# Performance work log

Measured on AMD Instinct MI355X. Metric: run time of the kernel, lower is better.

Reference implementation:

```python
import jax, jax.numpy as jnp
import numpy as np

N_NODES = 50000   # hypergraph nodes
N_EDGES = 20000   # hyperedges
M = 400000        # node-edge incidences (node copies)
L = 800000        # inner GIN graph edges per side
HID = 128
IN_DIM = 128
B = 32            # graphs in batch
C = 10            # num_classes
N_LAYERS = 2
INNER = 2         # inner_num_layers
BN_EPS = 1e-5


def setup_inputs() -> dict:
    key = jax.random.key(0)
    ks = jax.random.split(key, 16)
    s = 0.05
    inp = {}
    inp["x_N"] = jax.random.normal(ks[0], (N_NODES, IN_DIM), jnp.float32)
    # embedding linear
    inp["We"] = jax.random.normal(ks[1], (IN_DIM, HID), jnp.float32) * s
    inp["be"] = jnp.zeros((HID,), jnp.float32)
    # GIN params: [outer_layer, direction(N2E/E2N), inner_conv, mlp_linear, hid, hid]
    inp["Wg"] = jax.random.normal(ks[2], (N_LAYERS, 2, INNER, 2, HID, HID), jnp.float32) * s
    inp["bg"] = jnp.zeros((N_LAYERS, 2, INNER, 2, HID), jnp.float32)
    inp["eps_g"] = jnp.zeros((N_LAYERS, 2, INNER), jnp.float32)
    # eval-mode BatchNorm affine params per inner conv
    inp["gamma"] = jnp.ones((N_LAYERS, 2, INNER, HID), jnp.float32)
    inp["beta"] = jnp.zeros((N_LAYERS, 2, INNER, HID), jnp.float32)
    # per-layer prediction heads
    inp["Wp"] = jax.random.normal(ks[3], (N_LAYERS + 1, HID, C), jnp.float32) * s
    inp["bp"] = jnp.zeros((N_LAYERS + 1, C), jnp.float32)
    # index tensors
    inp["ori_node_idx"] = jax.random.randint(ks[4], (M,), 0, N_NODES)
    inp["node2edge"] = jax.random.randint(ks[5], (M,), 0, N_EDGES)
    inp["edge_index_N"] = jax.random.randint(ks[6], (2, L), 0, M)
    inp["ori_edge_idx"] = jax.random.randint(ks[7], (M,), 0, N_EDGES)
    inp["edge2node"] = jax.random.randint(ks[8], (M,), 0, N_NODES)
    inp["edge_index_E"] = jax.random.randint(ks[9], (2, L), 0, M)
    inp["batch"] = jax.random.randint(ks[10], (M,), 0, B)
    return inp


def _gin(x, src, dst, Wg, bg, eps, gamma, beta):
    # GIN over the copy graph: h = MLP((1+eps)*x + sum_{j->i} x_j), BN (eval), ReLU between convs
    inv_std = 1.0 / jnp.sqrt(1.0 + BN_EPS)
    n = x.shape[0]
    for l in range(INNER):
        agg = jax.ops.segment_sum(x[src], dst, num_segments=n)
        h = (1.0 + eps[l]) * x + agg
        h = jax.nn.relu(h @ Wg[l, 0] + bg[l, 0])
        h = h @ Wg[l, 1] + bg[l, 1]
        h = gamma[l] * h * inv_std + beta[l]
        x = jax.nn.relu(h) if l < INNER - 1 else h
    return x


def reference(x_N, We, be, Wg, bg, eps_g, gamma, beta, Wp, bp,
              ori_node_idx, node2edge, edge_index_N,
              ori_edge_idx, edge2node, edge_index_E, batch):
    node_x = x_N @ We + be                       # [N, HID]
    xs = [node_x]
    for i in range(N_LAYERS):
        # node -> edge: gather copies, inner GIN, segment-sum pool over hyperedges
        nx = node_x[ori_node_idx]                # [M, HID]
        nx = _gin(nx, edge_index_N[0], edge_index_N[1],
                  Wg[i, 0], bg[i, 0], eps_g[i, 0], gamma[i, 0], beta[i, 0])
        edge_x = jax.ops.segment_sum(nx, node2edge, num_segments=N_EDGES)
        edge_x = jax.nn.relu(edge_x)             # EdgeUpdate (dropout off in eval)
        # edge -> node
        ex = edge_x[ori_edge_idx]                # [M, HID]
        ex = _gin(ex, edge_index_E[0], edge_index_E[1],
                  Wg[i, 1], bg[i, 1], eps_g[i, 1], gamma[i, 1], beta[i, 1])
        node_x = jax.ops.segment_sum(ex, edge2node, num_segments=N_NODES)
        node_x = jax.nn.relu(node_x)             # NodeUpdate
        xs.append(node_x)
    score = jnp.zeros((B, C), x_N.dtype)
    for i, x in enumerate(xs):
        pooled = jax.ops.segment_sum(x[ori_node_idx], batch, num_segments=B)
        score = score + pooled @ Wp[i] + bp[i]
    return score
```

## Files before the change

kernel.cpp:

```cpp
#include <hip/hip_runtime.h>
#include <hip/hip_bf16.h>

#define HID 128
static const int N_NODES = 50000;
static const int N_EDGES = 20000;
static const int M_COPIES = 400000;
static const int L_EDGES = 800000;
static const int NBATCH = 32;
static const int NCLS = 10;
#define INV_STD 0.9999950000374997f
#define IDX_CAP 384
#define POOL_CAP 2048

typedef __attribute__((ext_vector_type(4))) float f32x4;
typedef __attribute__((ext_vector_type(8))) short short8;
typedef __attribute__((ext_vector_type(8))) unsigned short ushort8;
typedef __attribute__((ext_vector_type(4))) unsigned short u16x4;

__device__ __forceinline__ float bf2f(unsigned short u) {
    union { unsigned u; float f; } v; v.u = ((unsigned)u) << 16; return v.f;
}
__device__ __forceinline__ unsigned short f2bf(float f) {
    union { float f; unsigned u; } v; v.f = f;
    unsigned r = v.u + 0x7FFFu + ((v.u >> 16) & 1u);
    return (unsigned short)(r >> 16);
}
__device__ __forceinline__ void gatomic_add(float* p, float v) {
    unsafeAtomicAdd(p, v);
}

template<int H>
__device__ __forceinline__ void mfma_quarter(const unsigned short* Ws, const short8* xv,
                                             f32x4* acc, int quad, int ln) {
#pragma unroll
    for (int kc = 0; kc < 4; ++kc) {
#pragma unroll
        for (int tt = 0; tt < 2; ++tt) {
            short8 wa = *(const short8*)(Ws + (((kc * 4 + quad) * 32) + tt * 16 + ln) * 8);
            acc[H * 2 + tt] = __builtin_amdgcn_mfma_f32_16x16x32_bf16(wa, xv[kc], acc[H * 2 + tt], 0, 0, 0);
        }
    }
}

__global__ __launch_bounds__(256) void prep_w(const float* __restrict__ We,
                                              const float* __restrict__ Wg,
                                              unsigned short* __restrict__ Wt) {
    int t = blockIdx.x * 256 + threadIdx.x;
    if (t >= 17 * 16384) return;
    int mat = t >> 14, rem = t & 16383;
    int n = rem >> 7, k = rem & 127;
    const float* src = (mat == 0) ? We : (Wg + (size_t)(mat - 1) * 16384);
    Wt[t] = f2bf(src[k * 128 + n]);
}

__global__ __launch_bounds__(256) void hist_k(const int* __restrict__ idx, int n,
                                              int* __restrict__ cnt) {
    int t = blockIdx.x * 256 + threadIdx.x;
    if (t < n) atomicAdd(&cnt[idx[t]], 1);
}

__global__ __launch_bounds__(256) void scan1_k(int* __restrict__ a, int n,
                                               int* __restrict__ part) {
    __shared__ int s[256];
    int i = blockIdx.x * 256 + threadIdx.x;
    int v = (i < n) ? a[i] : 0;
    s[threadIdx.x] = v;
    __syncthreads();
#pragma unroll
    for (int d = 1; d < 256; d <<= 1) {
        int t = (threadIdx.x >= d) ? s[threadIdx.x - d] : 0;
        __syncthreads();
        s[threadIdx.x] += t;
        __syncthreads();
    }
    if (i < n) a[i] = s[threadIdx.x] - v;
    if (threadIdx.x == 255) part[blockIdx.x] = s[255];
}

__global__ __launch_bounds__(256) void scan2_k(int* __restrict__ part, int nb) {
    __shared__ int s[256];
    __shared__ int carry;
    if (threadIdx.x == 0) carry = 0;
    __syncthreads();
    for (int base = 0; base < nb; base += 256) {
        int i = base + threadIdx.x;
        int v = (i < nb) ? part[i] : 0;
        s[threadIdx.x] = v;
        __syncthreads();
#pragma unroll
        for (int d = 1; d < 256; d <<= 1) {
            int t = (threadIdx.x >= d) ? s[threadIdx.x - d] : 0;
            __syncthreads();
            s[threadIdx.x] += t;
            __syncthreads();
        }
        if (i < nb) part[i] = carry + s[threadIdx.x] - v;
        __syncthreads();
        if (threadIdx.x == 0) carry += s[255];
        __syncthreads();
    }
}

__global__ __launch_bounds__(256) void scan3_k(int* __restrict__ a, int n,
                                               const int* __restrict__ part) {
    int i = blockIdx.x * 256 + threadIdx.x;
    if (i < n) a[i] += part[blockIdx.x];
}

__global__ __launch_bounds__(256) void fill_edge_k(
    const int* __restrict__ src, const int* __restrict__ dst,
    const int* __restrict__ remap, int n, int* __restrict__ off,
    int* __restrict__ srcs, int* __restrict__ comps) {
    int e = blockIdx.x * 256 + threadIdx.x;
    if (e >= n) return;
    int d = dst[e];
    int pos = atomicAdd(&off[d], 1);
    int s = src[e];
    srcs[pos] = s;
    comps[pos] = remap[s];
}

__global__ __launch_bounds__(256) void fill_pool_k(
    const int* __restrict__ seg, int n, int* __restrict__ off,
    int* __restrict__ items) {
    int m = blockIdx.x * 256 + threadIdx.x;
    if (m >= n) return;
    int pos = atomicAdd(&off[seg[m]], 1);
    items[pos] = m;
}

__global__ __launch_bounds__(256) void segsum_pool(
    const unsigned* __restrict__ tbl, const int* __restrict__ off,
    const int* __restrict__ items, unsigned* __restrict__ out, int nseg)
{
    __shared__ int sIdx[POOL_CAP];
    int tid = threadIdx.x;
    int wave = tid >> 6, lane = tid & 63;
    int s0 = blockIdx.x * 16;
    int sN = min(s0 + 16, nseg);
    int bstart = (s0 == 0) ? 0 : off[s0 - 1];
    int bend = off[sN - 1];
    int cnt = bend - bstart;
    bool useLds = (cnt <= POOL_CAP);
    if (useLds)
        for (int i = tid; i < cnt; i += 256) sIdx[i] = items[bstart + i];
    __syncthreads();

    int mb = s0 + wave * 4;
    float a0[4] = {0.f, 0.f, 0.f, 0.f}, a1[4] = {0.f, 0.f, 0.f, 0.f};
    int pos[4], end[4];
#pragma unroll
    for (int i = 0; i < 4; ++i) {
        int m = mb + i;
        if (m < nseg) { pos[i] = (m == 0) ? 0 : off[m - 1]; end[i] = off[m]; }
        else { pos[i] = 0; end[i] = 0; }
    }
    bool more = (pos[0] < end[0]) | (pos[1] < end[1]) | (pos[2] < end[2]) | (pos[3] < end[3]);
    while (more) {
        more = false;
        unsigned v[4]; bool ld[4];
#pragma unroll
        for (int i = 0; i < 4; ++i) {
            ld[i] = pos[i] < end[i];
            if (ld[i]) {
                int r = useLds ? sIdx[pos[i] - bstart] : items[pos[i]];
                v[i] = tbl[(size_t)r * 64 + lane];
            }
        }
#pragma unroll
        for (int i = 0; i < 4; ++i) if (ld[i]) {
            a0[i] += bf2f((unsigned short)(v[i] & 0xffffu));
            a1[i] += bf2f((unsigned short)(v[i] >> 16));
            ++pos[i];
            more = more || (pos[i] < end[i]);
        }
    }
#pragma unroll
    for (int i = 0; i < 4; ++i) {
        int m = mb + i;
        if (m < nseg) {
            float r0 = fmaxf(a0[i], 0.f), r1 = fmaxf(a1[i], 0.f);
            out[(size_t)m * 64 + lane] = (unsigned)f2bf(r0) | ((unsigned)f2bf(r1) << 16);
        }
    }
}

template<bool CONV0>
__global__ __launch_bounds__(256, 6) void fused_conv(
    const unsigned short* __restrict__ tbl,
    const int* __restrict__ self_idx,
    const int* __restrict__ off, const int* __restrict__ items,
    const float* __restrict__ eps_ptr,
    const unsigned short* __restrict__ W1t, const float* __restrict__ b1,
    const unsigned short* __restrict__ W2t, const float* __restrict__ b2,
    const float* __restrict__ gam, const float* __restrict__ bet,
    unsigned short* __restrict__ out)
{
    __shared__ __align__(16) unsigned short Xs[16 * 64 * 8];
    __shared__ __align__(16) unsigned short Ws[16 * 32 * 8];
    __shared__ int sIdx[IDX_CAP];
    __shared__ int meta[192];
    const int tid = threadIdx.x;
    const int row0 = blockIdx.x * 64;

    const int bstart = (row0 == 0) ? 0 : off[row0 - 1];
    const int cnt = off[row0 + 63] - bstart;
    const bool useLds = (cnt <= IDX_CAP);

    if (tid < 64) {
        int gr = row0 + tid;
        meta[tid]       = (gr == 0) ? 0 : off[gr - 1];
        meta[64 + tid]  = off[gr];
        meta[128 + tid] = CONV0 ? self_idx[gr] : gr;
    }
#pragma unroll
    for (int i = 0; i < 2; ++i) {
        int chunk = tid + i * 256;
        int n = chunk >> 4, gg = chunk & 15;
        *(short8*)(Ws + (gg * 32 + n) * 8) = *(const short8*)(W1t + n * 128 + gg * 8);
    }
    if (useLds)
        for (int i = tid; i < cnt; i += 256) sIdx[i] = items[bstart + i];
    __syncthreads();

    const float e = 1.0f + eps_ptr[0];
    const int g = tid & 15;
    const int rb = tid >> 4;
#pragma unroll
    for (int i = 0; i < 4; ++i) {
        int r = rb + 16 * i;
        int start = meta[r], end = meta[64 + r], self = meta[128 + r];
        float a[8];
        ushort8 u = *(const ushort8*)(tbl + (size_t)self * 128 + g * 8);
#pragma unroll
        for (int j = 0; j < 8; ++j) a[j] = e * bf2f(u[j]);
        if (useLds) {
            int pos = start - bstart, pe = end - bstart;
            for (; pos + 2 <= pe; pos += 2) {
                int i0 = sIdx[pos], i1 = sIdx[pos + 1];
                ushort8 v0 = *(const ushort8*)(tbl + (size_t)i0 * 128 + g * 8);
                ushort8 v1 = *(const ushort8*)(tbl + (size_t)i1 * 128 + g * 8);
#pragma unroll
                for (int j = 0; j < 8; ++j) a[j] += bf2f(v0[j]) + bf2f(v1[j]);
            }
            if (pos < pe) {
                int i0 = sIdx[pos];
                ushort8 v0 = *(const ushort8*)(tbl + (size_t)i0 * 128 + g * 8);
#pragma unroll
                for (int j = 0; j < 8; ++j) a[j] += bf2f(v0[j]);
            }
        } else {
            for (int pos = start; pos < end; ++pos) {
                int rr = items[pos];
                ushort8 v = *(const ushort8*)(tbl + (size_t)rr * 128 + g * 8);
#pragma unroll
                for (int j = 0; j < 8; ++j) a[j] += bf2f(v[j]);
            }
        }
        ushort8 xv;
#pragma unroll
        for (int j = 0; j < 8; ++j) xv[j] = f2bf(a[j]);
        *(ushort8*)(Xs + (g * 64 + r) * 8) = xv;
    }
    __syncthreads();

    const int lane = tid & 63;
    const int ln = lane & 15, quad = lane >> 4;
    const int row = (tid >> 6) * 16 + ln;

    short8 xb[4];
#pragma unroll
    for (int kc = 0; kc < 4; ++kc)
        xb[kc] = *(const short8*)(Xs + ((kc * 4 + quad) * 64 + row) * 8);

    f32x4 acc[8];
#pragma unroll
    for (int t = 0; t < 8; ++t) acc[t] = (f32x4){0.f, 0.f, 0.f, 0.f};

    mfma_quarter<0>(Ws, xb, acc, quad, ln);
#pragma unroll
    for (int h = 1; h < 4; ++h) {
        __syncthreads();
#pragma unroll
        for (int i = 0; i < 2; ++i) {
            int chunk = tid + i * 256;
            int n = chunk >> 4, gg = chunk & 15;
            *(short8*)(Ws + (gg * 32 + n) * 8) = *(const short8*)(W1t + (h * 32 + n) * 128 + gg * 8);
        }
        __syncthreads();
        if (h == 1) mfma_quarter<1>(Ws, xb, acc, quad, ln);
        else if (h == 2) mfma_quarter<2>(Ws, xb, acc, quad, ln);
        else mfma_quarter<3>(Ws, xb, acc, quad, ln);
    }
    {
        const int j0 = (quad & 1) * 4;
#pragma unroll
        for (int t = 0; t < 8; ++t) {
            int p0 = t * 16 + quad * 4;
            f32x4 bv = *(const f32x4*)(b1 + p0);
            u16x4 hp;
#pragma unroll
            for (int i = 0; i < 4; ++i) hp[i] = f2bf(fmaxf(acc[t][i] + bv[i], 0.f));
            *(u16x4*)(Xs + ((p0 >> 3) * 64 + row) * 8 + j0) = hp;
        }
    }
    __syncthreads();
#pragma unroll
    for (int i = 0; i < 2; ++i) {
        int chunk = tid + i * 256;
        int n = chunk >> 4, gg = chunk & 15;
        *(short8*)(Ws + (gg * 32 + n) * 8) = *(const short8*)(W2t + n * 128 + gg * 8);
    }
    __syncthreads();

    short8 hb[4];
#pragma unroll
    for (int kc = 0; kc < 4; ++kc)
        hb[kc] = *(const short8*)(Xs + ((kc * 4 + quad) * 64 + row) * 8);

#pragma unroll
    for (int t = 0; t < 8; ++t) acc[t] = (f32x4){0.f, 0.f, 0.f, 0.f};

    mfma_quarter<0>(Ws, hb, acc, quad, ln);
#pragma unroll
    for (int h = 1; h < 4; ++h) {
        __syncthreads();
#pragma unroll
        for (int i = 0; i < 2; ++i) {
            int chunk = tid + i * 256;
            int n = chunk >> 4, gg = chunk & 15;
            *(short8*)(Ws + (gg * 32 + n) * 8) = *(const short8*)(W2t + (h * 32 + n) * 128 + gg * 8);
        }
        __syncthreads();
        if (h == 1) mfma_quarter<1>(Ws, hb, acc, quad, ln);
        else if (h == 2) mfma_quarter<2>(Ws, hb, acc, quad, ln);
        else mfma_quarter<3>(Ws, hb, acc, quad, ln);
    }

    const int m = row0 + row;
#pragma unroll
    for (int t = 0; t < 8; ++t) {
        int n0 = t * 16 + quad * 4;
        f32x4 bv = *(const f32x4*)(b2 + n0);
        f32x4 gv = *(const f32x4*)(gam + n0);
        f32x4 tv = *(const f32x4*)(bet + n0);
        u16x4 op;
#pragma unroll
        for (int i = 0; i < 4; ++i) {
            float h = acc[t][i] + bv[i];
            h = gv[i] * h * INV_STD + tv[i];
            if (CONV0) h = fmaxf(h, 0.f);
            op[i] = f2bf(h);
        }
        *(u16x4*)(out + (size_t)m * 128 + n0) = op;
    }
}

__global__ __launch_bounds__(256) void gemm_embed(
    const float* __restrict__ in, const unsigned short* __restrict__ Wt,
    const float* __restrict__ bias, unsigned short* __restrict__ out_bf, int rows)
{
    __shared__ __align__(16) unsigned short Xs[16 * 64 * 8];
    __shared__ __align__(16) unsigned short Ws[16 * 128 * 8];
    int tid = threadIdx.x;
    int row0 = blockIdx.x * 64;
#pragma unroll
    for (int i = 0; i < 8; ++i) {
        int chunk = tid + i * 256;
        int n = chunk >> 4, g = chunk & 15;
        *(short8*)(Ws + (g * 128 + n) * 8) = *(const short8*)(Wt + n * 128 + g * 8);
    }
#pragma unroll
    for (int i = 0; i < 4; ++i) {
        int chunk = tid + i * 256;
        int r = chunk >> 4, g = chunk & 15;
        int gr = row0 + r;
        ushort8 v;
        if (gr < rows) {
            const float* p = in + (size_t)gr * 128 + g * 8;
            f32x4 a0 = *(const f32x4*)p;
            f32x4 a1 = *(const f32x4*)(p + 4);
#pragma unroll
            for (int j = 0; j < 4; ++j) { v[j] = f2bf(a0[j]); v[4 + j] = f2bf(a1[j]); }
        } else {
#pragma unroll
            for (int j = 0; j < 8; ++j) v[j] = 0;
        }
        *(ushort8*)(Xs + (g * 64 + r) * 8) = v;
    }
    __syncthreads();
    int wave = tid >> 6, lane = tid & 63;
    int m0 = wave * 16;
    int ln = lane & 15, quad = lane >> 4;
    f32x4 acc[8];
#pragma unroll
    for (int t = 0; t < 8; ++t) acc[t] = (f32x4){0.f, 0.f, 0.f, 0.f};
#pragma unroll
    for (int kc = 0; kc < 4; ++kc) {
        int g = kc * 4 + quad;
        short8 a = *(const short8*)(Xs + (g * 64 + m0 + ln) * 8);
#pragma unroll
        for (int t = 0; t < 8; ++t) {
            short8 b = *(const short8*)(Ws + (g * 128 + t * 16 + ln) * 8);
            acc[t] = __builtin_amdgcn_mfma_f32_16x16x32_bf16(a, b, acc[t], 0, 0, 0);
        }
    }
#pragma unroll
    for (int t = 0; t < 8; ++t) {
        int col = t * 16 + ln;
        float bi = bias[col];
#pragma unroll
        for (int i = 0; i < 4; ++i) {
            int gr = row0 + m0 + quad * 4 + i;
            if (gr < rows) out_bf[(size_t)gr * 128 + col] = f2bf(acc[t][i] + bi);
        }
    }
}

template<bool ACCUM>
__global__ __launch_bounds__(256) void proj_y(
    const unsigned short* __restrict__ nx, const float* __restrict__ Wp,
    float* __restrict__ y, int rows)
{
    __shared__ float Wl[HID * NCLS];
    for (int i = threadIdx.x; i < HID * NCLS; i += 256) Wl[i] = Wp[i];
    __syncthreads();
    int r = blockIdx.x * 256 + threadIdx.x;
    if (r >= rows) return;
    float acc[NCLS];
#pragma unroll
    for (int c = 0; c < NCLS; ++c) acc[c] = 0.f;
    const unsigned short* xp = nx + (size_t)r * 128;
#pragma unroll 4
    for (int g = 0; g < 16; ++g) {
        ushort8 u = *(const ushort8*)(xp + g * 8);
#pragma unroll
        for (int j = 0; j < 8; ++j) {
            float xv = bf2f(u[j]);
            const float* w = Wl + (g * 8 + j) * NCLS;
#pragma unroll
            for (int c = 0; c < NCLS; ++c) acc[c] += xv * w[c];
        }
    }
    float* yp = y + (size_t)r * NCLS;
#pragma unroll
    for (int c = 0; c < NCLS; ++c) {
        if (ACCUM) yp[c] += acc[c];
        else yp[c] = acc[c];
    }
}

__global__ __launch_bounds__(256) void score_scatter(
    const float* __restrict__ y, const int* __restrict__ ori,
    const int* __restrict__ batch, float* __restrict__ score)
{
    __shared__ float sc[NBATCH * NCLS];
    for (int i = threadIdx.x; i < NBATCH * NCLS; i += 256) sc[i] = 0.f;
    __syncthreads();
    int stride = gridDim.x * 256;
    for (int m = blockIdx.x * 256 + threadIdx.x; m < M_COPIES; m += stride) {
        int r = ori[m], b = batch[m];
        const float* yp = y + (size_t)r * NCLS;
#pragma unroll
        for (int c = 0; c < NCLS; ++c)
            __hip_atomic_fetch_add(&sc[b * NCLS + c], yp[c],
                                   __ATOMIC_RELAXED, __HIP_MEMORY_SCOPE_WORKGROUP);
    }
    __syncthreads();
    for (int i = threadIdx.x; i < NBATCH * NCLS; i += 256) gatomic_add(score + i, sc[i]);
}

__global__ void score_final(const float* __restrict__ score, const float* __restrict__ bp,
                            float* __restrict__ out)
{
    int t = threadIdx.x;
    if (t >= NBATCH * NCLS) return;
    int c = t % NCLS;
    out[t] = score[t] + bp[c] + bp[NCLS + c] + bp[2 * NCLS + c];
}

__global__ void fill_sentinel(float* out, int n, float enc) {
    int t = blockIdx.x * 64 + threadIdx.x;
    if (t < n) out[t] = enc;
}

static inline void build_csr_edge(const int* src, const int* dst, const int* remap,
                                  int nitem, int nseg, int* off, int* part,
                                  int* srcs, int* comps, hipStream_t stream) {
    int nb = (nseg + 255) / 256;
    (void)hipMemsetAsync(off, 0, (size_t)nseg * 4, stream);
    hist_k<<<(nitem + 255) / 256, 256, 0, stream>>>(dst, nitem, off);
    scan1_k<<<nb, 256, 0, stream>>>(off, nseg, part);
    scan2_k<<<1, 256, 0, stream>>>(part, nb);
    scan3_k<<<nb, 256, 0, stream>>>(off, nseg, part);
    fill_edge_k<<<(nitem + 255) / 256, 256, 0, stream>>>(src, dst, remap, nitem, off, srcs, comps);
}
static inline void build_csr_pool(const int* seg, int nitem, int nseg,
                                  int* off, int* part, int* items, hipStream_t stream) {
    int nb = (nseg + 255) / 256;
    (void)hipMemsetAsync(off, 0, (size_t)nseg * 4, stream);
    hist_k<<<(nitem + 255) / 256, 256, 0, stream>>>(seg, nitem, off);
    scan1_k<<<nb, 256, 0, stream>>>(off, nseg, part);
    scan2_k<<<1, 256, 0, stream>>>(part, nb);
    scan3_k<<<nb, 256, 0, stream>>>(off, nseg, part);
    fill_pool_k<<<(nitem + 255) / 256, 256, 0, stream>>>(seg, nitem, off, items);
}

extern "C" void kernel_launch(void* const* d_in, const int* in_sizes, int n_in,
                              void* d_out, int out_size, void* d_ws, size_t ws_size,
                              hipStream_t stream) {
    const float* x_N    = (const float*)d_in[0];
    const float* We     = (const float*)d_in[1];
    const float* be     = (const float*)d_in[2];
    const float* Wg     = (const float*)d_in[3];
    const float* bg     = (const float*)d_in[4];
    const float* eps_g  = (const float*)d_in[5];
    const float* gam    = (const float*)d_in[6];
    const float* bet    = (const float*)d_in[7];
    const float* Wp     = (const float*)d_in[8];
    const float* bp     = (const float*)d_in[9];
    const int* ori_node = (const int*)d_in[10];
    const int* node2edge= (const int*)d_in[11];
    const int* eiN      = (const int*)d_in[12];
    const int* ori_edge = (const int*)d_in[13];
    const int* edge2node= (const int*)d_in[14];
    const int* eiE      = (const int*)d_in[15];
    const int* batch    = (const int*)d_in[16];

    char* p = (char*)d_ws;
    auto take = [&](size_t n) { char* r = p; p += (n + 255) & ~(size_t)255; return r; };
    unsigned short* Wt  = (unsigned short*)take((size_t)17 * 16384 * 2);
    unsigned short* Xb  = (unsigned short*)take((size_t)M_COPIES * 128 * 2);
    unsigned short* Xb2 = (unsigned short*)take((size_t)M_COPIES * 128 * 2);
    unsigned short* nx  = (unsigned short*)take((size_t)N_NODES * 128 * 2);
    unsigned short* ex  = (unsigned short*)take((size_t)N_EDGES * 128 * 2);
    float* y            = (float*)take((size_t)N_NODES * NCLS * 4);
    float* score        = (float*)take((size_t)NBATCH * NCLS * 4);
    int* offN           = (int*)take((size_t)M_COPIES * 4);
    int* offE           = (int*)take((size_t)M_COPIES * 4);
    int* off_n2e        = (int*)take((size_t)N_EDGES * 4);
    int* off_e2n        = (int*)take((size_t)N_NODES * 4);
    int* srcsN          = (int*)take((size_t)L_EDGES * 4);
    int* compsN         = (int*)take((size_t)L_EDGES * 4);
    int* srcsE          = (int*)take((size_t)L_EDGES * 4);
    int* compsE         = (int*)take((size_t)L_EDGES * 4);
    int* it_n2e         = (int*)take((size_t)M_COPIES * 4);
    int* it_e2n         = (int*)take((size_t)M_COPIES * 4);
    int* part           = (int*)take((size_t)2048 * 4);
    size_t need = (size_t)(p - (char*)d_ws);
    if (need > ws_size) {
        fill_sentinel<<<(out_size + 63) / 64, 64, 0, stream>>>(
            (float*)d_out, out_size, 1.0e9f + (float)ws_size);
        return;
    }

    prep_w<<<1088, 256, 0, stream>>>(We, Wg, Wt);
    (void)hipMemsetAsync(score, 0, (size_t)NBATCH * NCLS * 4, stream);

    build_csr_edge(eiN, eiN + L_EDGES, ori_node, L_EDGES, M_COPIES, offN, part, srcsN, compsN, stream);
    build_csr_edge(eiE, eiE + L_EDGES, ori_edge, L_EDGES, M_COPIES, offE, part, srcsE, compsE, stream);
    build_csr_pool(node2edge, M_COPIES, N_EDGES, off_n2e, part, it_n2e, stream);
    build_csr_pool(edge2node, M_COPIES, N_NODES, off_e2n, part, it_e2n, stream);

    gemm_embed<<<(N_NODES + 63) / 64, 256, 0, stream>>>(x_N, Wt, be, nx, N_NODES);
    proj_y<false><<<(N_NODES + 255) / 256, 256, 0, stream>>>(nx, Wp, y, N_NODES);

    const int MBLK = M_COPIES / 64;
    for (int layer = 0; layer < 2; ++layer) {
        for (int dir = 0; dir < 2; ++dir) {
            int cj0 = layer * 4 + dir * 2;
            int cj1 = cj0 + 1;
            const unsigned short* base = (dir == 0) ? nx : ex;
            const int* selfI = (dir == 0) ? ori_node : ori_edge;
            const int* offD  = (dir == 0) ? offN : offE;
            const int* srcsD = (dir == 0) ? srcsN : srcsE;
            const int* compD = (dir == 0) ? compsN : compsE;

            fused_conv<true><<<MBLK, 256, 0, stream>>>(
                base, selfI, offD, compD, eps_g + cj0,
                Wt + (size_t)(1 + cj0 * 2) * 16384, bg + (cj0 * 2) * 128,
                Wt + (size_t)(1 + cj0 * 2 + 1) * 16384, bg + (cj0 * 2 + 1) * 128,
                gam + cj0 * 128, bet + cj0 * 128, Xb);
            fused_conv<false><<<MBLK, 256, 0, stream>>>(
                Xb, nullptr, offD, srcsD, eps_g + cj1,
                Wt + (size_t)(1 + cj1 * 2) * 16384, bg + (cj1 * 2) * 128,
                Wt + (size_t)(1 + cj1 * 2 + 1) * 16384, bg + (cj1 * 2 + 1) * 128,
                gam + cj1 * 128, bet + cj1 * 128, Xb2);
            if (dir == 0) {
                segsum_pool<<<(N_EDGES + 15) / 16, 256, 0, stream>>>(
                    (const unsigned*)Xb2, off_n2e, it_n2e, (unsigned*)ex, N_EDGES);
            } else {
                segsum_pool<<<(N_NODES + 15) / 16, 256, 0, stream>>>(
                    (const unsigned*)Xb2, off_e2n, it_e2n, (unsigned*)nx, N_NODES);
                proj_y<true><<<(N_NODES + 255) / 256, 256, 0, stream>>>(
                    nx, Wp + (layer + 1) * HID * NCLS, y, N_NODES);
            }
        }
    }
    score_scatter<<<256, 256, 0, stream>>>(y, ori_node, batch, score);
    score_final<<<1, 320, 0, stream>>>(score, bp, (float*)d_out);
}
```

Before: 1.636 ms.

## Halve weight LDS tile in fused conv and rewrite segment pooling per-wave

The fused GIN conv kernel now stages weights in 16-column eighths instead of 32-column quarters. That halves the weight LDS buffer and raises the launch-bounds occupancy hint from 6 to 7 blocks, at the cost of twice as many barrier-separated reload steps. The segment-sum pooling kernel is rewritten so each wave owns one segment: four sub-groups stride over its items with 16-byte vector loads, then reduce with cross-lane shuffles. This drops the LDS index staging and the serial four-segment loop, aiming for better memory parallelism in the gather.

```diff
diff --git a/kernel.cpp b/kernel.cpp
--- a/kernel.cpp
+++ b/kernel.cpp
@@ -10,7 +10,6 @@
 static const int NCLS = 10;
 #define INV_STD 0.9999950000374997f
 #define IDX_CAP 384
-#define POOL_CAP 2048
 
 typedef __attribute__((ext_vector_type(4))) float f32x4;
 typedef __attribute__((ext_vector_type(8))) short short8;
@@ -30,15 +29,12 @@
 }
 
 template<int H>
-__device__ __forceinline__ void mfma_quarter(const unsigned short* Ws, const short8* xv,
-                                             f32x4* acc, int quad, int ln) {
+__device__ __forceinline__ void mfma_eighth(const unsigned short* Ws, const short8* xv,
+                                            f32x4* acc, int quad, int ln) {
 #pragma unroll
     for (int kc = 0; kc < 4; ++kc) {
-#pragma unroll
-        for (int tt = 0; tt < 2; ++tt) {
-            short8 wa = *(const short8*)(Ws + (((kc * 4 + quad) * 32) + tt * 16 + ln) * 8);
-            acc[H * 2 + tt] = __builtin_amdgcn_mfma_f32_16x16x32_bf16(wa, xv[kc], acc[H * 2 + tt], 0, 0, 0);
-        }
+        short8 wa = *(const short8*)(Ws + (((kc * 4 + quad) * 16) + ln) * 8);
+        acc[H] = __builtin_amdgcn_mfma_f32_16x16x32_bf16(wa, xv[kc], acc[H], 0, 0, 0);
     }
 }
 
@@ -130,63 +126,37 @@
 }
 
 __global__ __launch_bounds__(256) void segsum_pool(
-    const unsigned* __restrict__ tbl, const int* __restrict__ off,
-    const int* __restrict__ items, unsigned* __restrict__ out, int nseg)
+    const unsigned short* __restrict__ tbl, const int* __restrict__ off,
+    const int* __restrict__ items, unsigned short* __restrict__ out, int nseg)
 {
-    __shared__ int sIdx[POOL_CAP];
-    int tid = threadIdx.x;
-    int wave = tid >> 6, lane = tid & 63;
-    int s0 = blockIdx.x * 16;
-    int sN = min(s0 + 16, nseg);
-    int bstart = (s0 == 0) ? 0 : off[s0 - 1];
-    int bend = off[sN - 1];
-    int cnt = bend - bstart;
-    bool useLds = (cnt <= POOL_CAP);
-    if (useLds)
-        for (int i = tid; i < cnt; i += 256) sIdx[i] = items[bstart + i];
-    __syncthreads();
-
-    int mb = s0 + wave * 4;
-    float a0[4] = {0.f, 0.f, 0.f, 0.f}, a1[4] = {0.f, 0.f, 0.f, 0.f};
-    int pos[4], end[4];
-#pragma unroll
-    for (int i = 0; i < 4; ++i) {
-        int m = mb + i;
-        if (m < nseg) { pos[i] = (m == 0) ? 0 : off[m - 1]; end[i] = off[m]; }
-        else { pos[i] = 0; end[i] = 0; }
-    }
-    bool more = (pos[0] < end[0]) | (pos[1] < end[1]) | (pos[2] < end[2]) | (pos[3] < end[3]);
-    while (more) {
-        more = false;
-        unsigned v[4]; bool ld[4];
-#pragma unroll
-        for (int i = 0; i < 4; ++i) {
-            ld[i] = pos[i] < end[i];
-            if (ld[i]) {
-                int r = useLds ? sIdx[pos[i] - bstart] : items[pos[i]];
-                v[i] = tbl[(size_t)r * 64 + lane];
-            }
-        }
-#pragma unroll
-        for (int i = 0; i < 4; ++i) if (ld[i]) {
-            a0[i] += bf2f((unsigned short)(v[i] & 0xffffu));
-            a1[i] += bf2f((unsigned short)(v[i] >> 16));
-            ++pos[i];
-            more = more || (pos[i] < end[i]);
-        }
-    }
-#pragma unroll
-    for (int i = 0; i < 4; ++i) {
-        int m = mb + i;
-        if (m < nseg) {
-            float r0 = fmaxf(a0[i], 0.f), r1 = fmaxf(a1[i], 0.f);
-            out[(size_t)m * 64 + lane] = (unsigned)f2bf(r0) | ((unsigned)f2bf(r1) << 16);
-        }
+    int wave = threadIdx.x >> 6, lane = threadIdx.x & 63;
+    int seg = blockIdx.x * 4 + wave;
+    if (seg >= nseg) return;
+    int start = (seg == 0) ? 0 : off[seg - 1];
+    int end = off[seg];
+    int g = lane & 15, sub = lane >> 4;
+    float a[8] = {0.f, 0.f, 0.f, 0.f, 0.f, 0.f, 0.f, 0.f};
+    for (int p = start + sub; p < end; p += 4) {
+        int r = items[p];
+        ushort8 v = *(const ushort8*)(tbl + (size_t)r * 128 + g * 8);
+#pragma unroll
+        for (int j = 0; j < 8; ++j) a[j] += bf2f(v[j]);
+    }
+#pragma unroll
+    for (int j = 0; j < 8; ++j) {
+        a[j] += __shfl_xor(a[j], 16, 64);
+        a[j] += __shfl_xor(a[j], 32, 64);
+    }
+    if (sub == 0) {
+        ushort8 ov;
+#pragma unroll
+        for (int j = 0; j < 8; ++j) ov[j] = f2bf(fmaxf(a[j], 0.f));
+        *(ushort8*)(out + (size_t)seg * 128 + g * 8) = ov;
     }
 }
 
 template<bool CONV0>
-__global__ __launch_bounds__(256, 6) void fused_conv(
+__global__ __launch_bounds__(256, 7) void fused_conv(
     const unsigned short* __restrict__ tbl,
     const int* __restrict__ self_idx,
     const int* __restrict__ off, const int* __restrict__ items,
@@ -197,7 +167,7 @@
     unsigned short* __restrict__ out)
 {
     __shared__ __align__(16) unsigned short Xs[16 * 64 * 8];
-    __shared__ __align__(16) unsigned short Ws[16 * 32 * 8];
+    __shared__ __align__(16) unsigned short Ws[16 * 16 * 8];
     __shared__ int sIdx[IDX_CAP];
     __shared__ int meta[192];
     const int tid = threadIdx.x;
@@ -213,11 +183,9 @@
         meta[64 + tid]  = off[gr];
         meta[128 + tid] = CONV0 ? self_idx[gr] : gr;
     }
-#pragma unroll
-    for (int i = 0; i < 2; ++i) {
-        int chunk = tid + i * 256;
-        int n = chunk >> 4, gg = chunk & 15;
-        *(short8*)(Ws + (gg * 32 + n) * 8) = *(const short8*)(W1t + n * 128 + gg * 8);
+    {
+        int n = tid >> 4, gg = tid & 15;
+        *(short8*)(Ws + (gg * 16 + n) * 8) = *(const short8*)(W1t + n * 128 + gg * 8);
     }
     if (useLds)
         for (int i = tid; i < cnt; i += 256) sIdx[i] = items[bstart + i];
@@ -277,20 +245,24 @@
 #pragma unroll
     for (int t = 0; t < 8; ++t) acc[t] = (f32x4){0.f, 0.f, 0.f, 0.f};
 
-    mfma_quarter<0>(Ws, xb, acc, quad, ln);
-#pragma unroll
-    for (int h = 1; h < 4; ++h) {
-        __syncthreads();
-#pragma unroll
-        for (int i = 0; i < 2; ++i) {
-            int chunk = tid + i * 256;
-            int n = chunk >> 4, gg = chunk & 15;
-            *(short8*)(Ws + (gg * 32 + n) * 8) = *(const short8*)(W1t + (h * 32 + n) * 128 + gg * 8);
-        }
-        __syncthreads();
-        if (h == 1) mfma_quarter<1>(Ws, xb, acc, quad, ln);
-        else if (h == 2) mfma_quarter<2>(Ws, xb, acc, quad, ln);
-        else mfma_quarter<3>(Ws, xb, acc, quad, ln);
+    mfma_eighth<0>(Ws, xb, acc, quad, ln);
+#pragma unroll
+    for (int h = 1; h < 8; ++h) {
+        __syncthreads();
+        {
+            int n = tid >> 4, gg = tid & 15;
+            *(short8*)(Ws + (gg * 16 + n) * 8) = *(const short8*)(W1t + (h * 16 + n) * 128 + gg * 8);
+        }
+        __syncthreads();
+        switch (h) {
+            case 1: mfma_eighth<1>(Ws, xb, acc, quad, ln); break;
+            case 2: mfma_eighth<2>(Ws, xb, acc, quad, ln); break;
+            case 3: mfma_eighth<3>(Ws, xb, acc, quad, ln); break;
+            case 4: mfma_eighth<4>(Ws, xb, acc, quad, ln); break;
+            case 5: mfma_eighth<5>(Ws, xb, acc, quad, ln); break;
+            case 6: mfma_eighth<6>(Ws, xb, acc, quad, ln); break;
+            default: mfma_eighth<7>(Ws, xb, acc, quad, ln); break;
+        }
     }
     {
         const int j0 = (quad & 1) * 4;
@@ -305,11 +277,9 @@
         }
     }
     __syncthreads();
-#pragma unroll
-    for (int i = 0; i < 2; ++i) {
-        int chunk = tid + i * 256;
-        int n = chunk >> 4, gg = chunk & 15;
-        *(short8*)(Ws + (gg * 32 + n) * 8) = *(const short8*)(W2t + n * 128 + gg * 8);
+    {
+        int n = tid >> 4, gg = tid & 15;
+        *(short8*)(Ws + (gg * 16 + n) * 8) = *(const short8*)(W2t + n * 128 + gg * 8);
     }
     __syncthreads();
 
@@ -321,20 +291,24 @@
 #pragma unroll
     for (int t = 0; t < 8; ++t) acc[t] = (f32x4){0.f, 0.f, 0.f, 0.f};
 
-    mfma_quarter<0>(Ws, hb, acc, quad, ln);
-#pragma unroll
-    for (int h = 1; h < 4; ++h) {
-        __syncthreads();
-#pragma unroll
-        for (int i = 0; i < 2; ++i) {
-            int chunk = tid + i * 256;
-            int n = chunk >> 4, gg = chunk & 15;
-            *(short8*)(Ws + (gg * 32 + n) * 8) = *(const short8*)(W2t + (h * 32 + n) * 128 + gg * 8);
-        }
-        __syncthreads();
-        if (h == 1) mfma_quarter<1>(Ws, hb, acc, quad, ln);
-        else if (h == 2) mfma_quarter<2>(Ws, hb, acc, quad, ln);
-        else mfma_quarter<3>(Ws, hb, acc, quad, ln);
+    mfma_eighth<0>(Ws, hb, acc, quad, ln);
+#pragma unroll
+    for (int h = 1; h < 8; ++h) {
+        __syncthreads();
+        {
+            int n = tid >> 4, gg = tid & 15;
+            *(short8*)(Ws + (gg * 16 + n) * 8) = *(const short8*)(W2t + (h * 16 + n) * 128 + gg * 8);
+        }
+        __syncthreads();
+        switch (h) {
+            case 1: mfma_eighth<1>(Ws, hb, acc, quad, ln); break;
+            case 2: mfma_eighth<2>(Ws, hb, acc, quad, ln); break;
+            case 3: mfma_eighth<3>(Ws, hb, acc, quad, ln); break;
+            case 4: mfma_eighth<4>(Ws, hb, acc, quad, ln); break;
+            case 5: mfma_eighth<5>(Ws, hb, acc, quad, ln); break;
+            case 6: mfma_eighth<6>(Ws, hb, acc, quad, ln); break;
+            default: mfma_eighth<7>(Ws, hb, acc, quad, ln); break;
+        }
     }
 
     const int m = row0 + row;
@@ -587,11 +561,11 @@
                 Wt + (size_t)(1 + cj1 * 2 + 1) * 16384, bg + (cj1 * 2 + 1) * 128,
                 gam + cj1 * 128, bet + cj1 * 128, Xb2);
             if (dir == 0) {
-                segsum_pool<<<(N_EDGES + 15) / 16, 256, 0, stream>>>(
-                    (const unsigned*)Xb2, off_n2e, it_n2e, (unsigned*)ex, N_EDGES);
+                segsum_pool<<<(N_EDGES + 3) / 4, 256, 0, stream>>>(
+                    Xb2, off_n2e, it_n2e, ex, N_EDGES);
             } else {
-                segsum_pool<<<(N_NODES + 15) / 16, 256, 0, stream>>>(
-                    (const unsigned*)Xb2, off_e2n, it_e2n, (unsigned*)nx, N_NODES);
+                segsum_pool<<<(N_NODES + 3) / 4, 256, 0, stream>>>(
+                    Xb2, off_e2n, it_e2n, nx, N_NODES);
                 proj_y<true><<<(N_NODES + 255) / 256, 256, 0, stream>>>(
                     nx, Wp + (layer + 1) * HID * NCLS, y, N_NODES);
             }
```

New measurement: 1.527 ms. 6.7% less time.
